# Optimization experiments

Hardware: AMD Instinct MI355X
Metric: run time of the kernel (lower is better)

Reference implementation:

```python
import jax, jax.numpy as jnp
import numpy as np

B, P, S, D = 16, 512, 1024, 1024
H_FULL, H_LIGHT = 16, 8


def _mha(q, k, v, w_in, b_in, w_out, b_out, nh):
    # PyTorch nn.MultiheadAttention (batch_first=True), dropout=0 (eval).
    d = q.shape[-1]
    hd = d // nh
    wq, wk, wv = jnp.split(w_in, 3, axis=0)
    bq, bk, bv = jnp.split(b_in, 3, axis=0)

    def proj(x, w, b):
        return (x @ w.T + b).reshape(x.shape[0], x.shape[1], nh, hd)

    qh = proj(q, wq, bq)  # [B,Lq,H,hd]
    kh = proj(k, wk, bk)  # [B,Lk,H,hd]
    vh = proj(v, wv, bv)
    scale = 1.0 / jnp.sqrt(jnp.asarray(hd, q.dtype))
    scores = jnp.einsum('bqhd,bkhd->bhqk', qh, kh) * scale
    attn = jax.nn.softmax(scores, axis=-1)
    o = jnp.einsum('bhqk,bkhd->bqhd', attn, vh).reshape(q.shape[0], q.shape[1], d)
    out = o @ w_out.T + b_out
    return out, attn.mean(axis=1)  # avg weights over heads (torch default)


def _ln(x, g, b, eps=1e-5):
    mu = x.mean(-1, keepdims=True)
    var = ((x - mu) ** 2).mean(-1, keepdims=True)
    return (x - mu) / jnp.sqrt(var + eps) * g + b


def setup_inputs() -> dict:
    key = jax.random.key(0)
    ks = jax.random.split(key, 16)
    w = 0.02
    inp = {
        'proto': jax.random.normal(ks[0], (B, P, D), jnp.float32),
        'img_features': jax.random.normal(ks[1], (B, S, D), jnp.float32),
        'cross_w_in': jax.random.normal(ks[2], (3 * D, D), jnp.float32) * w,
        'cross_b_in': jnp.zeros((3 * D,), jnp.float32),
        'cross_w_out': jax.random.normal(ks[3], (D, D), jnp.float32) * w,
        'cross_b_out': jnp.zeros((D,), jnp.float32),
        'self_w_in': jax.random.normal(ks[4], (3 * D, D), jnp.float32) * w,
        'self_b_in': jnp.zeros((3 * D,), jnp.float32),
        'self_w_out': jax.random.normal(ks[5], (D, D), jnp.float32) * w,
        'self_b_out': jnp.zeros((D,), jnp.float32),
        'light_w_in': jax.random.normal(ks[6], (3 * D, D), jnp.float32) * w,
        'light_b_in': jnp.zeros((3 * D,), jnp.float32),
        'light_w_out': jax.random.normal(ks[7], (D, D), jnp.float32) * w,
        'light_b_out': jnp.zeros((D,), jnp.float32),
        'norm1_g': jnp.ones((D,), jnp.float32), 'norm1_b': jnp.zeros((D,), jnp.float32),
        'norm2_g': jnp.ones((D,), jnp.float32), 'norm2_b': jnp.zeros((D,), jnp.float32),
        'norm3_g': jnp.ones((D,), jnp.float32), 'norm3_b': jnp.zeros((D,), jnp.float32),
        'gate_w1': jax.random.normal(ks[8], (D, 3 * D), jnp.float32) * w,
        'gate_b1': jnp.zeros((D,), jnp.float32),
        'gate_w2': jax.random.normal(ks[9], (3, D), jnp.float32) * w,
        'gate_b2': jnp.zeros((3,), jnp.float32),
    }
    return inp


def reference(proto, img_features,
              cross_w_in, cross_b_in, cross_w_out, cross_b_out,
              self_w_in, self_b_in, self_w_out, self_b_out,
              light_w_in, light_b_in, light_w_out, light_b_out,
              norm1_g, norm1_b, norm2_g, norm2_b, norm3_g, norm3_b,
              gate_w1, gate_b1, gate_w2, gate_b2):
    cross_raw, attn_w = _mha(proto, img_features, img_features,
                             cross_w_in, cross_b_in, cross_w_out, cross_b_out, H_FULL)
    cross_out = _ln(proto + cross_raw, norm1_g, norm1_b)
    self_raw, _ = _mha(cross_out, cross_out, cross_out,
                       self_w_in, self_b_in, self_w_out, self_b_out, H_FULL)
    self_out = _ln(cross_out + self_raw, norm2_g, norm2_b)
    light_raw, _ = _mha(self_out, self_out, self_out,
                        light_w_in, light_b_in, light_w_out, light_b_out, H_LIGHT)
    light_out = _ln(self_out + light_raw, norm3_g, norm3_b)
    gate_in = jnp.concatenate([cross_out, self_out, light_out], axis=-1)  # [B,P,3D]
    h = jax.nn.gelu(gate_in @ gate_w1.T + gate_b1, approximate=False)
    gate_w = jax.nn.softmax(h @ gate_w2.T + gate_b2, axis=-1)  # [B,P,3]
    updated = (gate_w[..., 0:1] * cross_out
               + gate_w[..., 1:2] * self_out
               + gate_w[..., 2:3] * light_out)
    return updated, attn_w
```

## Files before the change

### kernel.cpp

```cpp
#include <hip/hip_runtime.h>
#include <hip/hip_bf16.h>

typedef __hip_bfloat16 bf16;
typedef __attribute__((ext_vector_type(8))) short short8;
typedef __attribute__((ext_vector_type(4))) float f32x4;

#define BD 16
#define PD 512
#define SD 1024
#define DD 1024

#define GLDS16(gp, lp)                                              \
  __builtin_amdgcn_global_load_lds(                                 \
      (const __attribute__((address_space(1))) void*)(gp),          \
      (__attribute__((address_space(3))) void*)(lp), 16, 0, 0)

__global__ __launch_bounds__(256) void f2b(const float* __restrict__ in,
                                           bf16* __restrict__ out, int n)
{
  int i = (blockIdx.x * 256 + threadIdx.x) * 4;
  if (i < n) {
    float4 v = *(const float4*)(in + i);
    out[i + 0] = __float2bfloat16(v.x);
    out[i + 1] = __float2bfloat16(v.y);
    out[i + 2] = __float2bfloat16(v.z);
    out[i + 3] = __float2bfloat16(v.w);
  }
}

__global__ __launch_bounds__(256) void gemm_nt(
    const bf16* __restrict__ A, int lda,
    const bf16* __restrict__ W, int ldw,
    const float* __restrict__ bias,
    bf16* __restrict__ C, int ldc,
    int K, int gelu)
{
  __shared__ bf16 As[3][128 * 32];
  __shared__ bf16 Bs[3][128 * 32];

  const int t = threadIdx.x;
  const int lane = t & 63, wv = t >> 6;
  const int m0 = blockIdx.y * 128;
  const int n0 = blockIdx.x * 128;
  const int rl = lane & 15, qd = lane >> 4;

  f32x4 acc[4][4];
  for (int i = 0; i < 4; i++)
    for (int j = 0; j < 4; j++)
      acc[i][j] = (f32x4){0.f, 0.f, 0.f, 0.f};

  const bf16* Ag = A + (size_t)(m0 + (t >> 2)) * lda + (t & 3) * 8;
  const bf16* Wg = W + (size_t)(n0 + (t >> 2)) * ldw + (t & 3) * 8;
  const size_t a_half = (size_t)64 * lda, w_half = (size_t)64 * ldw;
  const int lo = wv * 512;

  const int mw = (wv >> 1) * 64, nw = (wv & 1) * 64;

  const int nt = K >> 5;

#define STAGE(buf, k0)                          \
  do {                                          \
    GLDS16(Ag + (k0), &As[buf][lo]);            \
    GLDS16(Ag + a_half + (k0), &As[buf][2048 + lo]); \
    GLDS16(Wg + (k0), &Bs[buf][lo]);            \
    GLDS16(Wg + w_half + (k0), &Bs[buf][2048 + lo]); \
  } while (0)

  STAGE(0, 0);
  STAGE(1, 32);

  int cur = 0, pf = 2;
  for (int tt = 0; tt < nt; ++tt) {
    if (tt + 1 < nt) asm volatile("s_waitcnt vmcnt(4)" ::: "memory");
    else             asm volatile("s_waitcnt vmcnt(0)" ::: "memory");
    __builtin_amdgcn_s_barrier();
    if (tt + 2 < nt) STAGE(pf, (tt + 2) * 32);

    const bf16* Ac = As[cur];
    const bf16* Bc = Bs[cur];
    short8 a[4], b[4];
#pragma unroll
    for (int i = 0; i < 4; i++)
      a[i] = *(const short8*)&Ac[(mw + i * 16 + rl) * 32 + qd * 8];
#pragma unroll
    for (int j = 0; j < 4; j++)
      b[j] = *(const short8*)&Bc[(nw + j * 16 + rl) * 32 + qd * 8];
#pragma unroll
    for (int i = 0; i < 4; i++)
#pragma unroll
      for (int j = 0; j < 4; j++)
        acc[i][j] = __builtin_amdgcn_mfma_f32_16x16x32_bf16(a[i], b[j], acc[i][j], 0, 0, 0);

    cur = (cur == 2) ? 0 : cur + 1;
    pf  = (pf == 2) ? 0 : pf + 1;
  }
#undef STAGE

  for (int i = 0; i < 4; i++) {
    const int row = m0 + mw + i * 16 + qd * 4;
    for (int j = 0; j < 4; j++) {
      const int col = n0 + nw + j * 16 + rl;
      const float bv = bias[col];
      for (int r = 0; r < 4; r++) {
        float v = acc[i][j][r] + bv;
        if (gelu) v = 0.5f * v * (1.0f + erff(v * 0.70710678118654752f));
        C[(size_t)(row + r) * ldc + col] = __float2bfloat16(v);
      }
    }
  }
}

__global__ void transpose_v(const bf16* __restrict__ V, int ldv, int voff,
                            bf16* __restrict__ Vt, int L, int H, int hd)
{
  __shared__ float tile[32][33];
  const int bh = blockIdx.z;
  const int b = bh / H, h = bh % H;
  const int d0 = blockIdx.x * 32, s0 = blockIdx.y * 32;
  const int tx = threadIdx.x, ty = threadIdx.y;
  tile[ty][tx] = __bfloat162float(V[(size_t)(b * L + s0 + ty) * ldv + voff + h * hd + d0 + tx]);
  __syncthreads();
  Vt[(size_t)((b * H + h) * hd + d0 + ty) * L + s0 + tx] = __float2bfloat16(tile[tx][ty]);
}

template<int HD, bool STATS>
__global__ __launch_bounds__(256) void flash_attn(
    const bf16* __restrict__ Q, int ldq, int qoff,
    const bf16* __restrict__ Km, int ldk, int koff,
    const bf16* __restrict__ Vt,
    bf16* __restrict__ O, int ldo, int ooff,
    float* __restrict__ linv_out,
    int H, int Lq, int Lk, float scale)
{
  constexpr int KK = HD / 32;
  constexpr int NO = HD / 16;
  __shared__ __align__(16) __hip_bfloat16 pl[4][2][2][16][32];

  const int lane = threadIdx.x & 63, wv = threadIdx.x >> 6;
  const int rl = lane & 15, qd = lane >> 4;
  const int b = blockIdx.z, h = blockIdx.y;
  const int q0 = blockIdx.x * 128 + wv * 32;

  short8 qf[2][KK];
  for (int mt = 0; mt < 2; ++mt)
    for (int kk = 0; kk < KK; ++kk)
      qf[mt][kk] = *(const short8*)(Q + (size_t)(b * Lq + q0 + mt * 16 + rl) * ldq
                                      + qoff + h * HD + kk * 32 + qd * 8);

  const bf16* Kb = Km + (size_t)b * Lk * ldk + koff + h * HD + qd * 8;
  const bf16* Vb = Vt + (size_t)(b * H + h) * HD * Lk + qd * 8;

  float ls[2][4];
  for (int mt = 0; mt < 2; mt++)
    for (int r = 0; r < 4; r++) ls[mt][r] = 0.f;
  f32x4 oacc[2][NO];
  for (int mt = 0; mt < 2; mt++)
    for (int ni = 0; ni < NO; ni++) oacc[mt][ni] = (f32x4){0.f, 0.f, 0.f, 0.f};

  const int nS32 = Lk / 32;
  for (int i = 0; i < nS32; i++) {
    const int s0 = i * 32;
    for (int f = 0; f < 2; f++) {
      short8 kf[KK];
#pragma unroll
      for (int kk = 0; kk < KK; kk++)
        kf[kk] = *(const short8*)(Kb + (size_t)(s0 + f * 16 + rl) * ldk + kk * 32);
#pragma unroll
      for (int mt = 0; mt < 2; mt++) {
        f32x4 sc = (f32x4){0.f, 0.f, 0.f, 0.f};
#pragma unroll
        for (int kk = 0; kk < KK; kk++)
          sc = __builtin_amdgcn_mfma_f32_16x16x32_bf16(qf[mt][kk], kf[kk], sc, 0, 0, 0);
        for (int r = 0; r < 4; r++) {
          float p = __expf(sc[r] * scale);
          ls[mt][r] += p;
          pl[wv][i & 1][mt][qd * 4 + r][f * 16 + rl] = __float2bfloat16(p);
        }
      }
    }
    asm volatile("s_waitcnt lgkmcnt(0)" ::: "memory");
    short8 vf[NO];
#pragma unroll
    for (int ni = 0; ni < NO; ni++)
      vf[ni] = *(const short8*)(Vb + (size_t)(ni * 16 + rl) * Lk + s0);
#pragma unroll
    for (int mt = 0; mt < 2; mt++) {
      short8 pa = *(const short8*)&pl[wv][i & 1][mt][rl][qd * 8];
#pragma unroll
      for (int ni = 0; ni < NO; ni++)
        oacc[mt][ni] = __builtin_amdgcn_mfma_f32_16x16x32_bf16(pa, vf[ni], oacc[mt][ni], 0, 0, 0);
    }
  }

  float rinv[2][4];
  for (int mt = 0; mt < 2; mt++)
    for (int r = 0; r < 4; r++) {
      float v = ls[mt][r];
      for (int o = 1; o < 16; o <<= 1) v += __shfl_xor(v, o);
      rinv[mt][r] = 1.0f / v;
    }

  if (STATS) {
    if (rl == 0)
      for (int mt = 0; mt < 2; mt++)
        for (int r = 0; r < 4; r++)
          linv_out[((size_t)b * H + h) * Lq + q0 + mt * 16 + qd * 4 + r] = rinv[mt][r];
  }

  for (int mt = 0; mt < 2; mt++)
    for (int ni = 0; ni < NO; ni++)
      for (int r = 0; r < 4; r++)
        O[(size_t)(b * Lq + q0 + mt * 16 + qd * 4 + r) * ldo + ooff + h * HD + ni * 16 + rl]
            = __float2bfloat16(oacc[mt][ni][r] * rinv[mt][r]);
}

template<int HD>
__global__ __launch_bounds__(256) void probs_mean(
    const bf16* __restrict__ Q, int ldq, int qoff,
    const bf16* __restrict__ Km, int ldk, int koff,
    const float* __restrict__ linv, float* __restrict__ out_att,
    int H, int Lq, int Lk, float scale)
{
  constexpr int KK = HD / 32;
  const int lane = threadIdx.x & 63, wv = threadIdx.x >> 6;
  const int rl = lane & 15, qd = lane >> 4;
  const int b = blockIdx.z;
  const int q0 = blockIdx.x * 128 + wv * 32;
  const int s0 = blockIdx.y * 32;
  const float hs = 1.0f / 16.0f;

  f32x4 am[2][2];
  for (int mt = 0; mt < 2; mt++)
    for (int f = 0; f < 2; f++) am[mt][f] = (f32x4){0.f, 0.f, 0.f, 0.f};

  const bf16* Qb  = Q  + (size_t)(b * Lq + q0) * ldq + qoff + qd * 8;
  const bf16* Kb0 = Km + (size_t)(b * Lk + s0) * ldk + koff + qd * 8;
  const float* lb = linv + (size_t)b * H * Lq + q0 + qd * 4;

  for (int h = 0; h < H; h++) {
    short8 qf[2][KK], kf[2][KK];
#pragma unroll
    for (int mt = 0; mt < 2; mt++)
#pragma unroll
      for (int kk = 0; kk < KK; kk++)
        qf[mt][kk] = *(const short8*)(Qb + (size_t)(mt * 16 + rl) * ldq + h * HD + kk * 32);
#pragma unroll
    for (int f = 0; f < 2; f++)
#pragma unroll
      for (int kk = 0; kk < KK; kk++)
        kf[f][kk] = *(const short8*)(Kb0 + (size_t)(f * 16 + rl) * ldk + h * HD + kk * 32);
    float li[2][4];
#pragma unroll
    for (int mt = 0; mt < 2; mt++)
#pragma unroll
      for (int r = 0; r < 4; r++)
        li[mt][r] = lb[(size_t)h * Lq + mt * 16 + r];
#pragma unroll
    for (int mt = 0; mt < 2; mt++)
#pragma unroll
      for (int f = 0; f < 2; f++) {
        f32x4 sc = (f32x4){0.f, 0.f, 0.f, 0.f};
#pragma unroll
        for (int kk = 0; kk < KK; kk++)
          sc = __builtin_amdgcn_mfma_f32_16x16x32_bf16(qf[mt][kk], kf[f][kk], sc, 0, 0, 0);
#pragma unroll
        for (int r = 0; r < 4; r++)
          am[mt][f][r] += __expf(sc[r] * scale) * li[mt][r];
      }
  }

#pragma unroll
  for (int mt = 0; mt < 2; mt++)
#pragma unroll
    for (int f = 0; f < 2; f++)
#pragma unroll
      for (int r = 0; r < 4; r++)
        out_att[(size_t)(b * Lq + q0 + mt * 16 + qd * 4 + r) * Lk + s0 + f * 16 + rl]
            = am[mt][f][r] * hs;
}

template<bool XF32>
__global__ __launch_bounds__(256) void add_ln(
    const void* __restrict__ Xv, int ldx, int xoff,
    const bf16* __restrict__ Y,
    const float* __restrict__ g, const float* __restrict__ bb,
    bf16* __restrict__ out, int ldo, int ooff)
{
  const int row = blockIdx.x, t = threadIdx.x;
  const bf16* yr = Y + (size_t)row * 1024;
  float v[4], s = 0.f, s2 = 0.f;
  for (int i = 0; i < 4; i++) {
    int c = t * 4 + i;
    float xv;
    if (XF32) xv = ((const float*)Xv)[(size_t)row * ldx + xoff + c];
    else      xv = __bfloat162float(((const bf16*)Xv)[(size_t)row * ldx + xoff + c]);
    v[i] = xv + __bfloat162float(yr[c]);
    s += v[i]; s2 += v[i] * v[i];
  }
  __shared__ float red[2][4];
  for (int o = 32; o >= 1; o >>= 1) { s += __shfl_down(s, o); s2 += __shfl_down(s2, o); }
  const int wv = t >> 6, lane = t & 63;
  if (lane == 0) { red[0][wv] = s; red[1][wv] = s2; }
  __syncthreads();
  s  = red[0][0] + red[0][1] + red[0][2] + red[0][3];
  s2 = red[1][0] + red[1][1] + red[1][2] + red[1][3];
  const float mean = s * (1.0f / 1024.f);
  const float var = s2 * (1.0f / 1024.f) - mean * mean;
  const float rstd = rsqrtf(var + 1e-5f);
  for (int i = 0; i < 4; i++) {
    int c = t * 4 + i;
    float o = (v[i] - mean) * rstd * g[c] + bb[c];
    out[(size_t)row * ldo + ooff + c] = __float2bfloat16(o);
  }
}

__global__ __launch_bounds__(256) void gate_kernel(
    const bf16* __restrict__ Hb, const bf16* __restrict__ G,
    const float* __restrict__ w2, const float* __restrict__ b2,
    float* __restrict__ out)
{
  const int row = blockIdx.x, t = threadIdx.x;
  const bf16* hr = Hb + (size_t)row * 1024;
  float d0 = 0.f, d1 = 0.f, d2 = 0.f;
  for (int i = 0; i < 4; i++) {
    int c = t * 4 + i;
    float hv = __bfloat162float(hr[c]);
    d0 += hv * w2[c];
    d1 += hv * w2[1024 + c];
    d2 += hv * w2[2048 + c];
  }
  __shared__ float red[3][4];
  for (int o = 32; o >= 1; o >>= 1) {
    d0 += __shfl_down(d0, o); d1 += __shfl_down(d1, o); d2 += __shfl_down(d2, o);
  }
  const int wv = t >> 6, lane = t & 63;
  if (lane == 0) { red[0][wv] = d0; red[1][wv] = d1; red[2][wv] = d2; }
  __syncthreads();
  float l0 = red[0][0] + red[0][1] + red[0][2] + red[0][3] + b2[0];
  float l1 = red[1][0] + red[1][1] + red[1][2] + red[1][3] + b2[1];
  float l2 = red[2][0] + red[2][1] + red[2][2] + red[2][3] + b2[2];
  float mm = fmaxf(l0, fmaxf(l1, l2));
  float e0 = __expf(l0 - mm), e1 = __expf(l1 - mm), e2 = __expf(l2 - mm);
  float inv = 1.f / (e0 + e1 + e2);
  float g0 = e0 * inv, g1 = e1 * inv, g2 = e2 * inv;
  const bf16* gr = G + (size_t)row * 3072;
  for (int i = 0; i < 4; i++) {
    int c = t * 4 + i;
    float o = g0 * __bfloat162float(gr[c]) + g1 * __bfloat162float(gr[1024 + c])
            + g2 * __bfloat162float(gr[2048 + c]);
    out[(size_t)row * 1024 + c] = o;
  }
}

extern "C" void kernel_launch(void* const* d_in, const int* in_sizes, int n_in,
                              void* d_out, int out_size, void* d_ws, size_t ws_size,
                              hipStream_t stream)
{
  const float* proto = (const float*)d_in[0];
  const float* img   = (const float*)d_in[1];
  const float* c_wi  = (const float*)d_in[2];
  const float* c_bi  = (const float*)d_in[3];
  const float* c_wo  = (const float*)d_in[4];
  const float* c_bo  = (const float*)d_in[5];
  const float* s_wi  = (const float*)d_in[6];
  const float* s_bi  = (const float*)d_in[7];
  const float* s_wo  = (const float*)d_in[8];
  const float* s_bo  = (const float*)d_in[9];
  const float* l_wi  = (const float*)d_in[10];
  const float* l_bi  = (const float*)d_in[11];
  const float* l_wo  = (const float*)d_in[12];
  const float* l_bo  = (const float*)d_in[13];
  const float* n1g = (const float*)d_in[14]; const float* n1b = (const float*)d_in[15];
  const float* n2g = (const float*)d_in[16]; const float* n2b = (const float*)d_in[17];
  const float* n3g = (const float*)d_in[18]; const float* n3b = (const float*)d_in[19];
  const float* gw1 = (const float*)d_in[20]; const float* gb1 = (const float*)d_in[21];
  const float* gw2 = (const float*)d_in[22]; const float* gb2 = (const float*)d_in[23];

  float* out_upd = (float*)d_out;
  float* out_att = out_upd + (size_t)BD * PD * DD;

  char* ws = (char*)d_ws;
  bf16* WB = (bf16*)ws;
  bf16* w_cwi = WB + 0;
  bf16* w_cwo = WB + 3145728;
  bf16* w_swi = WB + 4194304;
  bf16* w_swo = WB + 7340032;
  bf16* w_lwi = WB + 8388608;
  bf16* w_lwo = WB + 11534336;
  bf16* w_gw1 = WB + 12582912;

  int bc = 16;
  while (bc > 1 && 31457280ull + (size_t)bc * 16777216ull > ws_size) bc >>= 1;

  char* pool = ws + 31457280;
  bf16*  Pb    = (bf16*)pool;
  bf16*  Ib    = (bf16*)(pool + (size_t)1048576 * bc);
  bf16*  G     = (bf16*)(pool + (size_t)3145728 * bc);
  bf16*  Vg    = (bf16*)(pool + (size_t)6291456 * bc);
  float* linvb = (float*)(pool + (size_t)6291456 * bc);
  bf16*  Bq    = (bf16*)(pool + (size_t)8388608 * bc);
  bf16*  Vt    = (bf16*)(pool + (size_t)11534336 * bc);
  bf16*  Qc    = (bf16*)(pool + (size_t)13631488 * bc);
  bf16*  AO    = (bf16*)(pool + (size_t)14680064 * bc);
  bf16*  OP    = (bf16*)(pool + (size_t)15728640 * bc);

  const dim3 blk(256);

  f2b<<<dim3(3072), blk, 0, stream>>>(c_wi, w_cwi, 3145728);
  f2b<<<dim3(1024), blk, 0, stream>>>(c_wo, w_cwo, 1048576);
  f2b<<<dim3(3072), blk, 0, stream>>>(s_wi, w_swi, 3145728);
  f2b<<<dim3(1024), blk, 0, stream>>>(s_wo, w_swo, 1048576);
  f2b<<<dim3(3072), blk, 0, stream>>>(l_wi, w_lwi, 3145728);
  f2b<<<dim3(1024), blk, 0, stream>>>(l_wo, w_lwo, 1048576);
  f2b<<<dim3(3072), blk, 0, stream>>>(gw1, w_gw1, 3145728);

  for (int b0 = 0; b0 < BD; b0 += bc) {
    const float* proto_c = proto + (size_t)b0 * PD * DD;
    const float* img_c   = img + (size_t)b0 * SD * DD;
    float* out_upd_c = out_upd + (size_t)b0 * PD * DD;
    float* out_att_c = out_att + (size_t)b0 * PD * SD;
    const int MP = bc * PD;
    const int MS = bc * SD;

    f2b<<<dim3(MP), blk, 0, stream>>>(proto_c, Pb, MP * DD);
    f2b<<<dim3(MS), blk, 0, stream>>>(img_c, Ib, MS * DD);

    gemm_nt<<<dim3(8, MP / 128), blk, 0, stream>>>(Pb, 1024, w_cwi, 1024, c_bi,
                                                   Qc, 1024, 1024, 0);
    gemm_nt<<<dim3(8, MS / 128), blk, 0, stream>>>(Ib, 1024, w_cwi + (size_t)1024 * 1024, 1024,
                                                   c_bi + 1024, Bq, 1024, 1024, 0);
    gemm_nt<<<dim3(8, MS / 128), blk, 0, stream>>>(Ib, 1024, w_cwi + (size_t)2048 * 1024, 1024,
                                                   c_bi + 2048, Vg, 1024, 1024, 0);
    transpose_v<<<dim3(2, 32, bc * 16), dim3(32, 32), 0, stream>>>(Vg, 1024, 0, Vt, 1024, 16, 64);
    flash_attn<64, true><<<dim3(4, 16, bc), blk, 0, stream>>>(
        Qc, 1024, 0, Bq, 1024, 0, Vt, AO, 1024, 0, linvb, 16, PD, SD, 0.125f);
    probs_mean<64><<<dim3(4, SD / 32, bc), blk, 0, stream>>>(
        Qc, 1024, 0, Bq, 1024, 0, linvb, out_att_c, 16, PD, SD, 0.125f);
    gemm_nt<<<dim3(8, MP / 128), blk, 0, stream>>>(AO, 1024, w_cwo, 1024, c_bo, OP, 1024, 1024, 0);
    add_ln<true><<<dim3(MP), blk, 0, stream>>>(proto_c, 1024, 0, OP, n1g, n1b, G, 3072, 0);

    gemm_nt<<<dim3(24, MP / 128), blk, 0, stream>>>(G, 3072, w_swi, 1024, s_bi, Bq, 3072, 1024, 0);
    transpose_v<<<dim3(2, 16, bc * 16), dim3(32, 32), 0, stream>>>(Bq, 3072, 2048, Vt, 512, 16, 64);
    flash_attn<64, false><<<dim3(4, 16, bc), blk, 0, stream>>>(
        Bq, 3072, 0, Bq, 3072, 1024, Vt, AO, 1024, 0, nullptr, 16, PD, PD, 0.125f);
    gemm_nt<<<dim3(8, MP / 128), blk, 0, stream>>>(AO, 1024, w_swo, 1024, s_bo, OP, 1024, 1024, 0);
    add_ln<false><<<dim3(MP), blk, 0, stream>>>(G, 3072, 0, OP, n2g, n2b, G, 3072, 1024);

    gemm_nt<<<dim3(24, MP / 128), blk, 0, stream>>>(G + 1024, 3072, w_lwi, 1024, l_bi,
                                                    Bq, 3072, 1024, 0);
    transpose_v<<<dim3(4, 16, bc * 8), dim3(32, 32), 0, stream>>>(Bq, 3072, 2048, Vt, 512, 8, 128);
    flash_attn<128, false><<<dim3(4, 8, bc), blk, 0, stream>>>(
        Bq, 3072, 0, Bq, 3072, 1024, Vt, AO, 1024, 0, nullptr, 8, PD, PD,
        0.08838834764831845f);
    gemm_nt<<<dim3(8, MP / 128), blk, 0, stream>>>(AO, 1024, w_lwo, 1024, l_bo, OP, 1024, 1024, 0);
    add_ln<false><<<dim3(MP), blk, 0, stream>>>(G, 3072, 1024, OP, n3g, n3b, G, 3072, 2048);

    gemm_nt<<<dim3(8, MP / 128), blk, 0, stream>>>(G, 3072, w_gw1, 3072, gb1, Qc, 1024, 3072, 1);
    gate_kernel<<<dim3(MP), blk, 0, stream>>>(Qc, G, gw2, gb2, out_upd_c);
  }
}
```

Measured before the change: 1.397 ms.

## Add 256x256 swizzled GEMM kernel and fuse K/V cross projections

After: 1.507 ms. +7.9%, slower.

```diff
diff --git a/kernel.cpp b/kernel.cpp
--- a/kernel.cpp
+++ b/kernel.cpp
@@ -49,12 +49,14 @@
     for (int j = 0; j < 4; j++)
       acc[i][j] = (f32x4){0.f, 0.f, 0.f, 0.f};
 
-  const bf16* Ag = A + (size_t)(m0 + (t >> 2)) * lda + (t & 3) * 8;
-  const bf16* Wg = W + (size_t)(n0 + (t >> 2)) * ldw + (t & 3) * 8;
+  const int scol = ((t & 3) ^ ((t >> 2) & 3)) * 8;
+  const bf16* Ag = A + (size_t)(m0 + (t >> 2)) * lda + scol;
+  const bf16* Wg = W + (size_t)(n0 + (t >> 2)) * ldw + scol;
   const size_t a_half = (size_t)64 * lda, w_half = (size_t)64 * ldw;
   const int lo = wv * 512;
 
   const int mw = (wv >> 1) * 64, nw = (wv & 1) * 64;
+  const int slo = rl & 3;
 
   const int nt = K >> 5;
 
@@ -81,10 +83,10 @@
     short8 a[4], b[4];
 #pragma unroll
     for (int i = 0; i < 4; i++)
-      a[i] = *(const short8*)&Ac[(mw + i * 16 + rl) * 32 + qd * 8];
+      a[i] = *(const short8*)&Ac[(mw + i * 16 + rl) * 32 + (qd ^ slo) * 8];
 #pragma unroll
     for (int j = 0; j < 4; j++)
-      b[j] = *(const short8*)&Bc[(nw + j * 16 + rl) * 32 + qd * 8];
+      b[j] = *(const short8*)&Bc[(nw + j * 16 + rl) * 32 + (qd ^ slo) * 8];
 #pragma unroll
     for (int i = 0; i < 4; i++)
 #pragma unroll
@@ -97,6 +99,93 @@
 #undef STAGE
 
   for (int i = 0; i < 4; i++) {
+    const int row = m0 + mw + i * 16 + qd * 4;
+    for (int j = 0; j < 4; j++) {
+      const int col = n0 + nw + j * 16 + rl;
+      const float bv = bias[col];
+      for (int r = 0; r < 4; r++) {
+        float v = acc[i][j][r] + bv;
+        if (gelu) v = 0.5f * v * (1.0f + erff(v * 0.70710678118654752f));
+        C[(size_t)(row + r) * ldc + col] = __float2bfloat16(v);
+      }
+    }
+  }
+}
+
+__global__ __launch_bounds__(512, 2) void gemm_nt256(
+    const bf16* __restrict__ A, int lda,
+    const bf16* __restrict__ W, int ldw,
+    const float* __restrict__ bias,
+    bf16* __restrict__ C, int ldc,
+    int K, int gelu)
+{
+  __shared__ bf16 As[2][256 * 64];
+  __shared__ bf16 Bs[2][256 * 64];
+
+  const int t = threadIdx.x;
+  const int lane = t & 63, wv = t >> 6;
+  const int rl = lane & 15, qd = lane >> 4;
+  const int m0 = blockIdx.y * 256;
+  const int n0 = blockIdx.x * 256;
+  const int mw = (wv >> 2) * 128, nw = (wv & 3) * 64;
+
+  f32x4 acc[8][4];
+#pragma unroll
+  for (int i = 0; i < 8; i++)
+#pragma unroll
+    for (int j = 0; j < 4; j++)
+      acc[i][j] = (f32x4){0.f, 0.f, 0.f, 0.f};
+
+  const int scol = ((t & 7) ^ ((t >> 3) & 7)) * 8;
+  const bf16* Ag = A + (size_t)(m0 + (t >> 3)) * lda + scol;
+  const bf16* Wg = W + (size_t)(n0 + (t >> 3)) * ldw + scol;
+
+#define STAGE256(buf, k0)                                              \
+  do {                                                                 \
+    _Pragma("unroll")                                                  \
+    for (int s = 0; s < 4; s++) {                                      \
+      GLDS16(Ag + (size_t)(s * 64) * lda + (k0), &As[buf][s * 4096 + wv * 512]); \
+      GLDS16(Wg + (size_t)(s * 64) * ldw + (k0), &Bs[buf][s * 4096 + wv * 512]); \
+    }                                                                  \
+  } while (0)
+
+  const int nt = K >> 6;
+  const int slo = rl & 7;
+
+  STAGE256(0, 0);
+
+  for (int tt = 0; tt < nt; ++tt) {
+    if (tt + 1 < nt) {
+      STAGE256((tt + 1) & 1, (tt + 1) * 64);
+      asm volatile("s_waitcnt vmcnt(8)" ::: "memory");
+    } else {
+      asm volatile("s_waitcnt vmcnt(0)" ::: "memory");
+    }
+    __builtin_amdgcn_s_barrier();
+
+    const bf16* Ac = As[tt & 1];
+    const bf16* Bc = Bs[tt & 1];
+#pragma unroll
+    for (int kk = 0; kk < 2; ++kk) {
+      const int cs = ((kk * 4 + qd) ^ slo) * 8;
+      short8 a[8], b[4];
+#pragma unroll
+      for (int i = 0; i < 8; i++)
+        a[i] = *(const short8*)&Ac[(mw + i * 16 + rl) * 64 + cs];
+#pragma unroll
+      for (int j = 0; j < 4; j++)
+        b[j] = *(const short8*)&Bc[(nw + j * 16 + rl) * 64 + cs];
+#pragma unroll
+      for (int i = 0; i < 8; i++)
+#pragma unroll
+        for (int j = 0; j < 4; j++)
+          acc[i][j] = __builtin_amdgcn_mfma_f32_16x16x32_bf16(a[i], b[j], acc[i][j], 0, 0, 0);
+    }
+    __builtin_amdgcn_s_barrier();
+  }
+#undef STAGE256
+
+  for (int i = 0; i < 8; i++) {
     const int row = m0 + mw + i * 16 + qd * 4;
     for (int j = 0; j < 4; j++) {
       const int col = n0 + nw + j * 16 + rl;
@@ -396,15 +485,16 @@
   bf16*  Pb    = (bf16*)pool;
   bf16*  Ib    = (bf16*)(pool + (size_t)1048576 * bc);
   bf16*  G     = (bf16*)(pool + (size_t)3145728 * bc);
-  bf16*  Vg    = (bf16*)(pool + (size_t)6291456 * bc);
-  float* linvb = (float*)(pool + (size_t)6291456 * bc);
+  bf16*  KVb   = (bf16*)(pool + (size_t)6291456 * bc);
   bf16*  Bq    = (bf16*)(pool + (size_t)8388608 * bc);
   bf16*  Vt    = (bf16*)(pool + (size_t)11534336 * bc);
   bf16*  Qc    = (bf16*)(pool + (size_t)13631488 * bc);
   bf16*  AO    = (bf16*)(pool + (size_t)14680064 * bc);
   bf16*  OP    = (bf16*)(pool + (size_t)15728640 * bc);
+  float* linvb = (float*)(pool + (size_t)15728640 * bc);
 
   const dim3 blk(256);
+  const dim3 blk512(512);
 
   f2b<<<dim3(3072), blk, 0, stream>>>(c_wi, w_cwi, 3145728);
   f2b<<<dim3(1024), blk, 0, stream>>>(c_wo, w_cwo, 1048576);
@@ -427,27 +517,26 @@
 
     gemm_nt<<<dim3(8, MP / 128), blk, 0, stream>>>(Pb, 1024, w_cwi, 1024, c_bi,
                                                    Qc, 1024, 1024, 0);
-    gemm_nt<<<dim3(8, MS / 128), blk, 0, stream>>>(Ib, 1024, w_cwi + (size_t)1024 * 1024, 1024,
-                                                   c_bi + 1024, Bq, 1024, 1024, 0);
-    gemm_nt<<<dim3(8, MS / 128), blk, 0, stream>>>(Ib, 1024, w_cwi + (size_t)2048 * 1024, 1024,
-                                                   c_bi + 2048, Vg, 1024, 1024, 0);
-    transpose_v<<<dim3(2, 32, bc * 16), dim3(32, 32), 0, stream>>>(Vg, 1024, 0, Vt, 1024, 16, 64);
+    gemm_nt256<<<dim3(8, MS / 256), blk512, 0, stream>>>(
+        Ib, 1024, w_cwi + (size_t)1024 * 1024, 1024, c_bi + 1024, KVb, 2048, 1024, 0);
+    transpose_v<<<dim3(2, 32, bc * 16), dim3(32, 32), 0, stream>>>(KVb, 2048, 1024, Vt, 1024, 16, 64);
     flash_attn<64, true><<<dim3(4, 16, bc), blk, 0, stream>>>(
-        Qc, 1024, 0, Bq, 1024, 0, Vt, AO, 1024, 0, linvb, 16, PD, SD, 0.125f);
+        Qc, 1024, 0, KVb, 2048, 0, Vt, AO, 1024, 0, linvb, 16, PD, SD, 0.125f);
     probs_mean<64><<<dim3(4, SD / 32, bc), blk, 0, stream>>>(
-        Qc, 1024, 0, Bq, 1024, 0, linvb, out_att_c, 16, PD, SD, 0.125f);
+        Qc, 1024, 0, KVb, 2048, 0, linvb, out_att_c, 16, PD, SD, 0.125f);
     gemm_nt<<<dim3(8, MP / 128), blk, 0, stream>>>(AO, 1024, w_cwo, 1024, c_bo, OP, 1024, 1024, 0);
     add_ln<true><<<dim3(MP), blk, 0, stream>>>(proto_c, 1024, 0, OP, n1g, n1b, G, 3072, 0);
 
-    gemm_nt<<<dim3(24, MP / 128), blk, 0, stream>>>(G, 3072, w_swi, 1024, s_bi, Bq, 3072, 1024, 0);
+    gemm_nt256<<<dim3(12, MP / 256), blk512, 0, stream>>>(
+        G, 3072, w_swi, 1024, s_bi, Bq, 3072, 1024, 0);
     transpose_v<<<dim3(2, 16, bc * 16), dim3(32, 32), 0, stream>>>(Bq, 3072, 2048, Vt, 512, 16, 64);
     flash_attn<64, false><<<dim3(4, 16, bc), blk, 0, stream>>>(
         Bq, 3072, 0, Bq, 3072, 1024, Vt, AO, 1024, 0, nullptr, 16, PD, PD, 0.125f);
     gemm_nt<<<dim3(8, MP / 128), blk, 0, stream>>>(AO, 1024, w_swo, 1024, s_bo, OP, 1024, 1024, 0);
     add_ln<false><<<dim3(MP), blk, 0, stream>>>(G, 3072, 0, OP, n2g, n2b, G, 3072, 1024);
 
-    gemm_nt<<<dim3(24, MP / 128), blk, 0, stream>>>(G + 1024, 3072, w_lwi, 1024, l_bi,
-                                                    Bq, 3072, 1024, 0);
+    gemm_nt256<<<dim3(12, MP / 256), blk512, 0, stream>>>(
+        G + 1024, 3072, w_lwi, 1024, l_bi, Bq, 3072, 1024, 0);
     transpose_v<<<dim3(4, 16, bc * 8), dim3(32, 32), 0, stream>>>(Bq, 3072, 2048, Vt, 512, 8, 128);
     flash_attn<128, false><<<dim3(4, 8, bc), blk, 0, stream>>>(
         Bq, 3072, 0, Bq, 3072, 1024, Vt, AO, 1024, 0, nullptr, 8, PD, PD,
@@ -455,7 +544,8 @@
     gemm_nt<<<dim3(8, MP / 128), blk, 0, stream>>>(AO, 1024, w_lwo, 1024, l_bo, OP, 1024, 1024, 0);
     add_ln<false><<<dim3(MP), blk, 0, stream>>>(G, 3072, 1024, OP, n3g, n3b, G, 3072, 2048);
 
-    gemm_nt<<<dim3(8, MP / 128), blk, 0, stream>>>(G, 3072, w_gw1, 3072, gb1, Qc, 1024, 3072, 1);
+    gemm_nt256<<<dim3(4, MP / 256), blk512, 0, stream>>>(
+        G, 3072, w_gw1, 3072, gb1, Qc, 1024, 3072, 1);
     gate_kernel<<<dim3(MP), blk, 0, stream>>>(Qc, G, gw2, gb2, out_upd_c);
   }
 }
```
